# Optimization experiments

Measured on AMD Instinct MI355X. Metric: run time of the kernel, lower is better.

The kernel has to match this reference:

```python
import jax, jax.numpy as jnp
import numpy as np

TOPK = 8
EPS = 1e-12  # matches torch F.normalize default eps


def setup_inputs() -> dict:
    key = jax.random.key(0)
    x = jax.random.normal(key, (8, 2048, 128), dtype=jnp.float32)
    return {"x": x}


def reference(x) -> jnp.ndarray:
    B, N, D = x.shape
    # --- pairwise dot scores on L2-normalized features (cosine similarity) ---
    norm = jnp.sqrt(jnp.sum(x * x, axis=-1, keepdims=True))
    normed = x / jnp.maximum(norm, EPS)
    scores = jnp.einsum('bnd,bmd->bnm', normed, normed)  # [B, N, N]

    # --- top-k per row -> binary adjacency via scatter ---
    _, idx = jax.lax.top_k(scores, TOPK)  # [B, N, k]
    bi = jnp.arange(B)[:, None, None]
    ni = jnp.arange(N)[None, :, None]
    adj = jnp.zeros((B, N, N), dtype=x.dtype).at[bi, ni, idx].set(1.0)

    # --- symmetrize and add self loops ---
    adj = jnp.maximum(adj, jnp.swapaxes(adj, 1, 2))
    eye = jnp.eye(N, dtype=x.dtype)
    adj = jnp.maximum(adj, eye[None, :, :])
    return adj
```

## Files before the change

kernel.cpp:

```cpp
#include <hip/hip_runtime.h>
#include <cstdint>

#define NN 2048
#define DD 128
#define BATCH 8
#define NROWS 16384
#define MARGIN 0.02f
#define CAP2 48

typedef __attribute__((ext_vector_type(8))) short bf16x8;
typedef __attribute__((ext_vector_type(4))) float f32x4;
typedef unsigned long long u64;
typedef unsigned int u32;
typedef unsigned short u16;

__device__ __forceinline__ u32 bf16rne(float f) {
  u32 u = __float_as_uint(f);
  return (u + 0x7fffu + ((u >> 16) & 1u)) >> 16;
}

__global__ __launch_bounds__(256) void k_normalize(const float* __restrict__ x,
                                                   double* __restrict__ rinv,
                                                   u32* __restrict__ nb) {
  const int wave = threadIdx.x >> 6, lane = threadIdx.x & 63;
  const long long row = (long long)blockIdx.x * 4 + wave;
  float2 v = ((const float2*)(x + row * DD))[lane];
  const double d0 = v.x, d1 = v.y;
  double s = d0 * d0 + d1 * d1;
  #pragma unroll
  for (int m = 32; m >= 1; m >>= 1) s += __shfl_xor(s, m, 64);
  double den = sqrt(s); den = den > 1e-12 ? den : 1e-12;
  if (lane == 0) rinv[row] = 1.0 / den;
  double2 o; o.x = d0 / den; o.y = d1 / den;
  nb[row * (DD / 2) + lane] = bf16rne((float)o.x) | (bf16rne((float)o.y) << 16);
}

#define CXF(i, j) { const float a_ = L[i], b_ = L[j]; L[i] = fmaxf(a_, b_); L[j] = fminf(a_, b_); }
__device__ __forceinline__ void merge8f(float (&kv)[8], const float (&ov)[8]) {
  float L[8];
  #pragma unroll
  for (int i = 0; i < 8; ++i) L[i] = fmaxf(kv[i], ov[7 - i]);
  CXF(0, 4) CXF(1, 5) CXF(2, 6) CXF(3, 7)
  CXF(0, 2) CXF(1, 3) CXF(4, 6) CXF(5, 7)
  CXF(0, 1) CXF(2, 3) CXF(4, 5) CXF(6, 7)
  #pragma unroll
  for (int i = 0; i < 8; ++i) kv[i] = L[i];
}

__device__ __forceinline__ u64 make_key(double s, int col) {
  u64 u = (u64)__double_as_longlong(s);
  const u64 m = (u64)((long long)u >> 63);
  u ^= (m | 0x8000000000000000ull);
  return (u & ~2047ull) | (u64)(2047 - col);
}
__device__ __forceinline__ u64 umax64(u64 a, u64 b) { return a > b ? a : b; }
__device__ __forceinline__ u64 umin64(u64 a, u64 b) { return a > b ? b : a; }
__device__ __forceinline__ void merge8(u64 (&kv)[8], const u64 (&ov)[8]) {
  u64 L[8];
  #pragma unroll
  for (int i = 0; i < 8; ++i) L[i] = umax64(kv[i], ov[7 - i]);
#define CX(i, j) { const u64 a_ = L[i], b_ = L[j]; L[i] = umax64(a_, b_); L[j] = umin64(a_, b_); }
  CX(0, 4) CX(1, 5) CX(2, 6) CX(3, 7)
  CX(0, 2) CX(1, 3) CX(4, 6) CX(5, 7)
  CX(0, 1) CX(2, 3) CX(4, 5) CX(6, 7)
#undef CX
  #pragma unroll
  for (int i = 0; i < 8; ++i) kv[i] = L[i];
}
__device__ __forceinline__ void insert8u(u64 (&v)[8], u64 nk) {
  if (nk > v[7]) {
    v[7] = nk;
    #pragma unroll
    for (int q = 7; q >= 1; --q) {
      const u64 a = v[q - 1], b = v[q];
      const bool sw = b > a;
      v[q - 1] = sw ? b : a; v[q] = sw ? a : b;
    }
  }
}

__global__ __launch_bounds__(256) void k_gram_bmax(const u32* __restrict__ nb,
                                                   u16* __restrict__ bmaxg,
                                                   float4* __restrict__ outz) {
  __shared__ u16 bml[4][64][16];
  const int tid = threadIdx.x; const int w = tid >> 6; const int l = tid & 63;
  const int q = l >> 4; const int m = l & 15;
  const f32x4 z4 = {0.0f, 0.0f, 0.0f, 0.0f};
  const int rowblk = blockIdx.x >> 2; const int split = blockIdx.x & 3;
  const int row0 = rowblk * 64;
  const int b = rowblk >> 5;
  const int c0w = split * 512 + w * 128;
  const u32* Bb = nb + ((long long)b * NN + c0w) * (DD / 2);

  bf16x8 ar4[4][4];
  #pragma unroll
  for (int rf = 0; rf < 4; ++rf) {
    const u32* Ap = nb + (long long)(row0 + 16 * rf + m) * (DD / 2) + 4 * q;
    #pragma unroll
    for (int cc = 0; cc < 4; ++cc) ar4[rf][cc] = *(const bf16x8*)(Ap + 16 * cc);
  }
  bf16x8 bcA[4], bcB[4];

#define LOADB(DST, T) { const u32* p_ = Bb + (long long)(16 * (T) + m) * (DD / 2) + 4 * q; \
  _Pragma("unroll") for (int cc = 0; cc < 4; ++cc) DST[cc] = *(const bf16x8*)(p_ + 16 * cc); }
#define TILE1(BC, T) {                                                             \
    _Pragma("unroll") for (int rf = 0; rf < 4; ++rf) {                             \
      f32x4 acc = z4;                                                              \
      _Pragma("unroll") for (int cc = 0; cc < 4; ++cc)                             \
        acc = __builtin_amdgcn_mfma_f32_16x16x32_bf16(BC[cc], ar4[rf][cc], acc, 0, 0, 0); \
      float bm_ = fmaxf(fmaxf(acc[0], acc[1]), fmaxf(acc[2], acc[3]));             \
      bm_ = fmaxf(bm_, __shfl_xor(bm_, 16, 64));                                   \
      bm_ = fmaxf(bm_, __shfl_xor(bm_, 32, 64));                                   \
      if (q == 0) bml[w][16 * rf + m][T] = (u16)bf16rne(bm_);                      \
    } }

  LOADB(bcA, 0)
  #pragma unroll
  for (int t = 0; t < 8; t += 2) {
    LOADB(bcB, t + 1)
    TILE1(bcA, t)
    if (t + 2 < 8) LOADB(bcA, t + 2)
    TILE1(bcB, t + 1)
  }
#undef LOADB
#undef TILE1

  {
    const uint4 v = *(const uint4*)&bml[w][l][0];
    *(uint4*)(bmaxg + ((long long)split * 16384 + row0 + l) * 32 + w * 8) = v;
  }

  {
    const int base = blockIdx.x * 256 + tid;
    const float4 zf = {0.0f, 0.0f, 0.0f, 0.0f};
    #pragma unroll 8
    for (int k = 0; k < 32; ++k) outz[base + k * 262144] = zf;
  }
}

__global__ __launch_bounds__(512) void k_topk_fused(const u32* __restrict__ nb,
                                                    const u16* __restrict__ bmaxg,
                                                    const float* __restrict__ x,
                                                    const double* __restrict__ rinv,
                                                    float* __restrict__ out) {
  __shared__ float thl[64];
  __shared__ u32 cnt[64];
  __shared__ u32 cand[64][CAP2];

  const int tid = threadIdx.x; const int w = tid >> 6; const int l = tid & 63;
  const int q = l >> 4; const int m = l & 15;
  const int s_ = q, idx_ = m;
  const int rowblk = blockIdx.x;
  const int row0 = rowblk * 64;
  const int b = rowblk >> 5;
  const long long brow = (long long)b * NN;

  bf16x8 pvals = {0,0,0,0,0,0,0,0}, pones = {0,0,0,0,0,0,0,0};
  if (q == 0) {
    pvals[0] = (short)(__float_as_uint((float)(m + 1)) >> 16);
    pones[0] = (short)(__float_as_uint(1.0f) >> 16);
  }
  const f32x4 z4 = {0.0f, 0.0f, 0.0f, 0.0f};
  const f32x4 pr  = __builtin_amdgcn_mfma_f32_16x16x32_bf16(pvals, pones, z4, 0, 0, 0);
  const f32x4 pr2 = __builtin_amdgcn_mfma_f32_16x16x32_bf16(pones, pvals, z4, 0, 0, 0);
  int cof[4];
  #pragma unroll
  for (int p = 0; p < 4; ++p) cof[p] = (int)pr[p] - 1;
  const int rof = (int)pr2[0] - 1;

  if (tid < 64) cnt[tid] = 0u;

  for (int j = 0; j < 8; ++j) {
    const int rib = w * 8 + j;
    const int row = row0 + rib;
    const u32 bm2 = *(const u32*)(bmaxg + ((long long)s_ * 16384 + row) * 32 + 2 * idx_);
    const float b0 = __uint_as_float(bm2 << 16);
    const float b1 = __uint_as_float(bm2 & 0xFFFF0000u);
    float mx = fmaxf(b0, b1);
    float kv8[8];
    {
      const float o  = __shfl_xor(mx, 1, 64);
      const float h2 = fmaxf(mx, o), l2 = fminf(mx, o);
      const float p0 = __shfl_xor(h2, 2, 64), p1 = __shfl_xor(l2, 2, 64);
      const float m0 = fmaxf(h2, p0);
      const float xx = fminf(h2, p0);
      const float yy = fmaxf(l2, p1);
      const float m3 = fminf(l2, p1);
      const float m1 = fmaxf(xx, yy);
      const float m2 = fminf(xx, yy);
      const float q0 = __shfl_xor(m0, 4, 64), q1 = __shfl_xor(m1, 4, 64);
      const float q2 = __shfl_xor(m2, 4, 64), q3 = __shfl_xor(m3, 4, 64);
      float L[8] = {m0, m1, m2, m3, q3, q2, q1, q0};
      CXF(0, 4) CXF(1, 5) CXF(2, 6) CXF(3, 7)
      CXF(0, 2) CXF(1, 3) CXF(4, 6) CXF(5, 7)
      CXF(0, 1) CXF(2, 3) CXF(4, 5) CXF(6, 7)
      #pragma unroll
      for (int s = 0; s < 8; ++s) kv8[s] = L[s];
      #pragma unroll
      for (int mk = 8; mk <= 32; mk <<= 1) {
        float ov[8];
        #pragma unroll
        for (int s = 0; s < 8; ++s) ov[s] = __shfl_xor(kv8[s], mk, 64);
        merge8f(kv8, ov);
      }
    }
    if (l == 0) thl[rib] = kv8[7] - MARGIN;
  }
  __syncthreads();

  float th4[4]; int rib4[4];
  #pragma unroll
  for (int rf = 0; rf < 4; ++rf) {
    rib4[rf] = 16 * rf + rof;
    th4[rf] = thl[rib4[rf]];
  }

  const int c0w = w * 256;
  const u32* Bb = nb + (brow + c0w) * (DD / 2);
  bf16x8 ar4[4][4];
  #pragma unroll
  for (int rf = 0; rf < 4; ++rf) {
    const u32* Ap = nb + (long long)(row0 + 16 * rf + m) * (DD / 2) + 4 * q;
    #pragma unroll
    for (int cc = 0; cc < 4; ++cc) ar4[rf][cc] = *(const bf16x8*)(Ap + 16 * cc);
  }
  bf16x8 bcA[4], bcB[4];

#define LOADB2(DST, T) { const u32* p_ = Bb + (long long)(16 * (T) + m) * (DD / 2) + 4 * q; \
  _Pragma("unroll") for (int cc = 0; cc < 4; ++cc) DST[cc] = *(const bf16x8*)(p_ + 16 * cc); }
#define TILEF(BC, T) {                                                             \
    _Pragma("unroll") for (int rf = 0; rf < 4; ++rf) {                             \
      f32x4 acc = z4;                                                              \
      _Pragma("unroll") for (int cc = 0; cc < 4; ++cc)                             \
        acc = __builtin_amdgcn_mfma_f32_16x16x32_bf16(BC[cc], ar4[rf][cc], acc, 0, 0, 0); \
      _Pragma("unroll") for (int p = 0; p < 4; ++p) {                              \
        if (acc[p] >= th4[rf]) {                                                   \
          const u32 id = atomicAdd(&cnt[rib4[rf]], 1u);                            \
          if (id < CAP2) cand[rib4[rf]][id] = (u32)(c0w + 16 * (T) + cof[p]);      \
        }                                                                          \
      }                                                                            \
    } }

  LOADB2(bcA, 0)
  #pragma unroll
  for (int t = 0; t < 16; t += 2) {
    LOADB2(bcB, t + 1)
    TILEF(bcA, t)
    if (t + 2 < 16) LOADB2(bcA, t + 2)
    TILEF(bcB, t + 1)
  }
#undef LOADB2
#undef TILEF
  __syncthreads();

  for (int j = 0; j < 8; ++j) {
    const int rib = w * 8 + j;
    const int r = row0 + rib;
    const int n = r & (NN - 1);
    const int c = (int)cnt[rib];
    const double ri = rinv[r];
    u64 kv[8];
    #pragma unroll
    for (int s = 0; s < 8; ++s) kv[s] = 0ull;

    if (c <= CAP2) {
      float2 a4[4];
      #pragma unroll
      for (int jj = 0; jj < 4; ++jj)
        a4[jj] = ((const float2*)(x + (long long)r * DD))[idx_ + 16 * jj];

      for (int i = 0; i < c; i += 4) {
        const int gi = i + s_;
        const bool valid = gi < c;
        const int col = valid ? (int)cand[rib][gi] : 0;
        const float2* cp = (const float2*)(x + (brow + col) * DD);
        double d = 0.0;
        #pragma unroll
        for (int jj = 0; jj < 4; ++jj) {
          const float2 bv = cp[idx_ + 16 * jj];
          d = fma((double)a4[jj].x, (double)bv.x, d);
          d = fma((double)a4[jj].y, (double)bv.y, d);
        }
        #pragma unroll
        for (int mk = 1; mk <= 8; mk <<= 1) d += __shfl_xor(d, mk, 64);
        if (valid) insert8u(kv, make_key(d * ri * rinv[brow + col], col));
      }
      #pragma unroll
      for (int mk = 16; mk <= 32; mk <<= 1) {
        u64 ov[8];
        #pragma unroll
        for (int s = 0; s < 8; ++s) ov[s] = __shfl_xor(kv[s], mk, 64);
        merge8(kv, ov);
      }
    } else {
      for (int base = 0; base < NN; base += 64) {
        const int col = base + l;
        const float* ap = x + (long long)r * DD;
        const float* cp2 = x + (brow + col) * DD;
        double d = 0.0;
        for (int kk = 0; kk < 64; ++kk) {
          const float2 av = ((const float2*)ap)[kk];
          const float2 bv = ((const float2*)cp2)[kk];
          d = fma((double)av.x, (double)bv.x, fma((double)av.y, (double)bv.y, d));
        }
        d = d * ri * rinv[brow + col];
        u64 one[8];
        one[0] = make_key(d, col);
        #pragma unroll
        for (int s = 1; s < 8; ++s) one[s] = 0ull;
        #pragma unroll
        for (int mk = 1; mk <= 32; mk <<= 1) {
          u64 ov[8];
          #pragma unroll
          for (int s = 0; s < 8; ++s) ov[s] = __shfl_xor(one[s], mk, 64);
          merge8(one, ov);
        }
        merge8(kv, one);
      }
    }

    const long long orow = (long long)r * NN;
    const long long obase = brow * NN;
    if (l == 8) out[orow + n] = 1.0f;
    #pragma unroll
    for (int s = 0; s < 8; ++s) {
      const int mcol = 2047 - (int)(kv[s] & 2047ull);
      if (l == s) {
        out[orow + mcol] = 1.0f;
        out[obase + (long long)mcol * NN + n] = 1.0f;
      }
    }
  }
}

extern "C" void kernel_launch(void* const* d_in, const int* in_sizes, int n_in,
                              void* d_out, int out_size, void* d_ws, size_t ws_size,
                              hipStream_t stream) {
  const float* x = (const float*)d_in[0];
  float* out = (float*)d_out;
  char* ws = (char*)d_ws;
  u32* nb = (u32*)ws;
  double* rinv = (double*)(ws + 4194304);
  u16* bmaxg = (u16*)(ws + 4325376);

  hipLaunchKernelGGL(k_normalize, dim3(NROWS / 4), dim3(256), 0, stream, x, rinv, nb);
  hipLaunchKernelGGL(k_gram_bmax, dim3(1024), dim3(256), 0, stream, nb, bmaxg,
                     (float4*)out);
  hipLaunchKernelGGL(k_topk_fused, dim3(256), dim3(512), 0, stream, nb, bmaxg, x, rinv, out);
}
```

Baseline: 243.7 us.

## Fuse block-max Gram pass into top-k kernel and move output zeroing to normalize

Merges the separate block-max Gram kernel into the top-k kernel. Each 1024-thread block now computes per-tile maxima for its 64 rows across all 2048 columns into shared memory as fp32, removing the global bmaxg round trip and one launch. The zero-fill of the output moves into the normalize kernel. In exchange, the grid is only 256 large blocks, which lowers parallelism for the Gram pass that previously ran on 1024 blocks, and the larger shared-memory footprint may cut occupancy.

```diff
diff --git a/kernel.cpp b/kernel.cpp
--- a/kernel.cpp
+++ b/kernel.cpp
@@ -21,7 +21,8 @@
 
 __global__ __launch_bounds__(256) void k_normalize(const float* __restrict__ x,
                                                    double* __restrict__ rinv,
-                                                   u32* __restrict__ nb) {
+                                                   u32* __restrict__ nb,
+                                                   float4* __restrict__ outz) {
   const int wave = threadIdx.x >> 6, lane = threadIdx.x & 63;
   const long long row = (long long)blockIdx.x * 4 + wave;
   float2 v = ((const float2*)(x + row * DD))[lane];
@@ -33,6 +34,13 @@
   if (lane == 0) rinv[row] = 1.0 / den;
   double2 o; o.x = d0 / den; o.y = d1 / den;
   nb[row * (DD / 2) + lane] = bf16rne((float)o.x) | (bf16rne((float)o.y) << 16);
+
+  {
+    const int base = blockIdx.x * 256 + threadIdx.x;
+    const float4 zf = {0.0f, 0.0f, 0.0f, 0.0f};
+    #pragma unroll
+    for (int k = 0; k < 8; ++k) outz[base + k * 1048576] = zf;
+  }
 }
 
 #define CXF(i, j) { const float a_ = L[i], b_ = L[j]; L[i] = fmaxf(a_, b_); L[j] = fminf(a_, b_); }
@@ -79,18 +87,36 @@
   }
 }
 
-__global__ __launch_bounds__(256) void k_gram_bmax(const u32* __restrict__ nb,
-                                                   u16* __restrict__ bmaxg,
-                                                   float4* __restrict__ outz) {
-  __shared__ u16 bml[4][64][16];
+__global__ __launch_bounds__(1024) void k_build(const u32* __restrict__ nb,
+                                                const float* __restrict__ x,
+                                                const double* __restrict__ rinv,
+                                                float* __restrict__ out) {
+  __shared__ float bmf[64][130];
+  __shared__ float thl[64];
+  __shared__ u32 cnt[64];
+  __shared__ u32 cand[64][CAP2];
+
   const int tid = threadIdx.x; const int w = tid >> 6; const int l = tid & 63;
   const int q = l >> 4; const int m = l & 15;
-  const f32x4 z4 = {0.0f, 0.0f, 0.0f, 0.0f};
-  const int rowblk = blockIdx.x >> 2; const int split = blockIdx.x & 3;
+  const int rowblk = blockIdx.x;
   const int row0 = rowblk * 64;
   const int b = rowblk >> 5;
-  const int c0w = split * 512 + w * 128;
-  const u32* Bb = nb + ((long long)b * NN + c0w) * (DD / 2);
+  const long long brow = (long long)b * NN;
+
+  bf16x8 pvals = {0,0,0,0,0,0,0,0}, pones = {0,0,0,0,0,0,0,0};
+  if (q == 0) {
+    pvals[0] = (short)(__float_as_uint((float)(m + 1)) >> 16);
+    pones[0] = (short)(__float_as_uint(1.0f) >> 16);
+  }
+  const f32x4 z4 = {0.0f, 0.0f, 0.0f, 0.0f};
+  const f32x4 pr  = __builtin_amdgcn_mfma_f32_16x16x32_bf16(pvals, pones, z4, 0, 0, 0);
+  const f32x4 pr2 = __builtin_amdgcn_mfma_f32_16x16x32_bf16(pones, pvals, z4, 0, 0, 0);
+  int cof[4];
+  #pragma unroll
+  for (int p = 0; p < 4; ++p) cof[p] = (int)pr[p] - 1;
+  const int rof = (int)pr2[0] - 1;
+
+  if (tid < 64) cnt[tid] = 0u;
 
   bf16x8 ar4[4][4];
   #pragma unroll
@@ -99,10 +125,14 @@
     #pragma unroll
     for (int cc = 0; cc < 4; ++cc) ar4[rf][cc] = *(const bf16x8*)(Ap + 16 * cc);
   }
+
+  const int c0w = w * 128;
+  const u32* Bb = nb + (brow + c0w) * (DD / 2);
   bf16x8 bcA[4], bcB[4];
 
 #define LOADB(DST, T) { const u32* p_ = Bb + (long long)(16 * (T) + m) * (DD / 2) + 4 * q; \
   _Pragma("unroll") for (int cc = 0; cc < 4; ++cc) DST[cc] = *(const bf16x8*)(p_ + 16 * cc); }
+
 #define TILE1(BC, T) {                                                             \
     _Pragma("unroll") for (int rf = 0; rf < 4; ++rf) {                             \
       f32x4 acc = z4;                                                              \
@@ -111,7 +141,7 @@
       float bm_ = fmaxf(fmaxf(acc[0], acc[1]), fmaxf(acc[2], acc[3]));             \
       bm_ = fmaxf(bm_, __shfl_xor(bm_, 16, 64));                                   \
       bm_ = fmaxf(bm_, __shfl_xor(bm_, 32, 64));                                   \
-      if (q == 0) bml[w][16 * rf + m][T] = (u16)bf16rne(bm_);                      \
+      if (q == 0) bmf[16 * rf + m][w * 8 + (T)] = bm_;                             \
     } }
 
   LOADB(bcA, 0)
@@ -122,60 +152,13 @@
     if (t + 2 < 8) LOADB(bcA, t + 2)
     TILE1(bcB, t + 1)
   }
-#undef LOADB
 #undef TILE1
-
-  {
-    const uint4 v = *(const uint4*)&bml[w][l][0];
-    *(uint4*)(bmaxg + ((long long)split * 16384 + row0 + l) * 32 + w * 8) = v;
-  }
-
-  {
-    const int base = blockIdx.x * 256 + tid;
-    const float4 zf = {0.0f, 0.0f, 0.0f, 0.0f};
-    #pragma unroll 8
-    for (int k = 0; k < 32; ++k) outz[base + k * 262144] = zf;
-  }
-}
-
-__global__ __launch_bounds__(512) void k_topk_fused(const u32* __restrict__ nb,
-                                                    const u16* __restrict__ bmaxg,
-                                                    const float* __restrict__ x,
-                                                    const double* __restrict__ rinv,
-                                                    float* __restrict__ out) {
-  __shared__ float thl[64];
-  __shared__ u32 cnt[64];
-  __shared__ u32 cand[64][CAP2];
-
-  const int tid = threadIdx.x; const int w = tid >> 6; const int l = tid & 63;
-  const int q = l >> 4; const int m = l & 15;
-  const int s_ = q, idx_ = m;
-  const int rowblk = blockIdx.x;
-  const int row0 = rowblk * 64;
-  const int b = rowblk >> 5;
-  const long long brow = (long long)b * NN;
-
-  bf16x8 pvals = {0,0,0,0,0,0,0,0}, pones = {0,0,0,0,0,0,0,0};
-  if (q == 0) {
-    pvals[0] = (short)(__float_as_uint((float)(m + 1)) >> 16);
-    pones[0] = (short)(__float_as_uint(1.0f) >> 16);
-  }
-  const f32x4 z4 = {0.0f, 0.0f, 0.0f, 0.0f};
-  const f32x4 pr  = __builtin_amdgcn_mfma_f32_16x16x32_bf16(pvals, pones, z4, 0, 0, 0);
-  const f32x4 pr2 = __builtin_amdgcn_mfma_f32_16x16x32_bf16(pones, pvals, z4, 0, 0, 0);
-  int cof[4];
-  #pragma unroll
-  for (int p = 0; p < 4; ++p) cof[p] = (int)pr[p] - 1;
-  const int rof = (int)pr2[0] - 1;
-
-  if (tid < 64) cnt[tid] = 0u;
-
-  for (int j = 0; j < 8; ++j) {
-    const int rib = w * 8 + j;
-    const int row = row0 + rib;
-    const u32 bm2 = *(const u32*)(bmaxg + ((long long)s_ * 16384 + row) * 32 + 2 * idx_);
-    const float b0 = __uint_as_float(bm2 << 16);
-    const float b1 = __uint_as_float(bm2 & 0xFFFF0000u);
+  __syncthreads();
+
+  for (int j = 0; j < 4; ++j) {
+    const int rib = w * 4 + j;
+    const float b0 = bmf[rib][2 * l];
+    const float b1 = bmf[rib][2 * l + 1];
     float mx = fmaxf(b0, b1);
     float kv8[8];
     {
@@ -215,19 +198,6 @@
     th4[rf] = thl[rib4[rf]];
   }
 
-  const int c0w = w * 256;
-  const u32* Bb = nb + (brow + c0w) * (DD / 2);
-  bf16x8 ar4[4][4];
-  #pragma unroll
-  for (int rf = 0; rf < 4; ++rf) {
-    const u32* Ap = nb + (long long)(row0 + 16 * rf + m) * (DD / 2) + 4 * q;
-    #pragma unroll
-    for (int cc = 0; cc < 4; ++cc) ar4[rf][cc] = *(const bf16x8*)(Ap + 16 * cc);
-  }
-  bf16x8 bcA[4], bcB[4];
-
-#define LOADB2(DST, T) { const u32* p_ = Bb + (long long)(16 * (T) + m) * (DD / 2) + 4 * q; \
-  _Pragma("unroll") for (int cc = 0; cc < 4; ++cc) DST[cc] = *(const bf16x8*)(p_ + 16 * cc); }
 #define TILEF(BC, T) {                                                             \
     _Pragma("unroll") for (int rf = 0; rf < 4; ++rf) {                             \
       f32x4 acc = z4;                                                              \
@@ -241,20 +211,20 @@
       }                                                                            \
     } }
 
-  LOADB2(bcA, 0)
-  #pragma unroll
-  for (int t = 0; t < 16; t += 2) {
-    LOADB2(bcB, t + 1)
+  LOADB(bcA, 0)
+  #pragma unroll
+  for (int t = 0; t < 8; t += 2) {
+    LOADB(bcB, t + 1)
     TILEF(bcA, t)
-    if (t + 2 < 16) LOADB2(bcA, t + 2)
+    if (t + 2 < 8) LOADB(bcA, t + 2)
     TILEF(bcB, t + 1)
   }
-#undef LOADB2
 #undef TILEF
+#undef LOADB
   __syncthreads();
 
-  for (int j = 0; j < 8; ++j) {
-    const int rib = w * 8 + j;
+  for (int j = 0; j < 4; ++j) {
+    const int rib = w * 4 + j;
     const int r = row0 + rib;
     const int n = r & (NN - 1);
     const int c = (int)cnt[rib];
@@ -267,17 +237,17 @@
       float2 a4[4];
       #pragma unroll
       for (int jj = 0; jj < 4; ++jj)
-        a4[jj] = ((const float2*)(x + (long long)r * DD))[idx_ + 16 * jj];
+        a4[jj] = ((const float2*)(x + (long long)r * DD))[m + 16 * jj];
 
       for (int i = 0; i < c; i += 4) {
-        const int gi = i + s_;
+        const int gi = i + q;
         const bool valid = gi < c;
         const int col = valid ? (int)cand[rib][gi] : 0;
         const float2* cp = (const float2*)(x + (brow + col) * DD);
         double d = 0.0;
         #pragma unroll
         for (int jj = 0; jj < 4; ++jj) {
-          const float2 bv = cp[idx_ + 16 * jj];
+          const float2 bv = cp[m + 16 * jj];
           d = fma((double)a4[jj].x, (double)bv.x, d);
           d = fma((double)a4[jj].y, (double)bv.y, d);
         }
@@ -341,10 +311,8 @@
   char* ws = (char*)d_ws;
   u32* nb = (u32*)ws;
   double* rinv = (double*)(ws + 4194304);
-  u16* bmaxg = (u16*)(ws + 4325376);
-
-  hipLaunchKernelGGL(k_normalize, dim3(NROWS / 4), dim3(256), 0, stream, x, rinv, nb);
-  hipLaunchKernelGGL(k_gram_bmax, dim3(1024), dim3(256), 0, stream, nb, bmaxg,
+
+  hipLaunchKernelGGL(k_normalize, dim3(NROWS / 4), dim3(256), 0, stream, x, rinv, nb,
                      (float4*)out);
-  hipLaunchKernelGGL(k_topk_fused, dim3(256), dim3(512), 0, stream, nb, bmaxg, x, rinv, out);
-}
+  hipLaunchKernelGGL(k_build, dim3(256), dim3(1024), 0, stream, nb, x, rinv, out);
+}
```

Result: faster. 228.6 us (-6.2%).
